# Kernel tuning notes

Measured on AMD Instinct MI355X. Metric: run time of the kernel, lower is better.

The kernel has to match this reference:

```python
import jax, jax.numpy as jnp
import numpy as np

B, S, D, H, F, V, T, L = 64, 1024, 256, 256, 128, 50000, 64, 8
H2 = 2 * H
DIN = H2 + D + 3 * F  # 1152


def setup_inputs() -> dict:
    key = jax.random.key(0)
    ks = jax.random.split(key, 12)
    sd = 0.05
    return {
        "word_ids": jax.random.randint(ks[0], (B, S), 1, V, dtype=jnp.int32),
        "embed": jax.random.normal(ks[1], (V, D), jnp.float32) * sd,
        "encoder_outputs": jax.random.normal(ks[2], (B, S, H2), jnp.float32) * sd,
        "wconv1": jax.random.normal(ks[3], (F, 1, D), jnp.float32) * sd,
        "bconv1": jax.random.normal(ks[4], (F,), jnp.float32) * sd,
        "wconv2": jax.random.normal(ks[5], (F, 2, D), jnp.float32) * sd,
        "bconv2": jax.random.normal(ks[6], (F,), jnp.float32) * sd,
        "wconv3": jax.random.normal(ks[7], (F, 3, D), jnp.float32) * sd,
        "bconv3": jax.random.normal(ks[8], (F,), jnp.float32) * sd,
        "W_ih": jax.random.normal(ks[9], (4 * H2, DIN), jnp.float32) * sd,
        "W_hh": jax.random.normal(ks[10], (4 * H2, H2), jnp.float32) * sd,
        "W_fc": jax.random.normal(ks[11], (T, H2), jnp.float32) * sd,
        "seg_len": L,
    }


def reference(word_ids, embed, encoder_outputs, wconv1, bconv1, wconv2, bconv2,
              wconv3, bconv3, W_ih, W_hh, W_fc, seg_len):
    b, s = word_ids.shape
    d = embed.shape[1]
    h2 = encoder_outputs.shape[-1]
    h = h2 // 2
    nseg = s // seg_len

    # word features via embedding lookup (WordFeature with single 'word' feature)
    wf = embed[word_ids]                                  # [B, S, D]
    xs = wf.reshape(b, nseg, seg_len, d)                  # [B, nseg, L, D]
    c_w = xs.mean(axis=2)                                 # [B, nseg, D]
    es = encoder_outputs.reshape(b, nseg, seg_len, h2)
    c_h = es.mean(axis=2)                                 # [B, nseg, 2H]

    # char-CNN per segment: conv2d(1->F, (fs, D)) == 1D conv over time with D in-channels
    xc = xs.reshape(b * nseg, seg_len, d).transpose(0, 2, 1)  # [N, D, L]

    def conv_pool(w, bias):
        k = w.transpose(0, 2, 1)                          # [F, D, fs]
        y = jax.lax.conv_general_dilated(xc, k, window_strides=(1,),
                                         padding="VALID",
                                         dimension_numbers=("NCH", "OIH", "NCH"))
        y = jax.nn.relu(y + bias[None, :, None])
        return y.max(axis=2)                              # max-pool over time -> [N, F]

    c_x = jnp.concatenate([conv_pool(wconv1, bconv1),
                           conv_pool(wconv2, bconv2),
                           conv_pool(wconv3, bconv3)], axis=1)
    c_x = c_x.reshape(b, nseg, -1)                        # [B, nseg, 3F]

    dec_in = jnp.concatenate([c_w, c_h, c_x], axis=-1)    # [B, nseg, DIN]

    # decoder init: fwd-last / bwd-first encoder states
    h0 = jnp.concatenate([encoder_outputs[:, -1, :h], encoder_outputs[:, 0, h:]], axis=1)
    c0 = jnp.zeros_like(h0)

    def step(carry, x):
        hh, cc = carry
        gates = x @ W_ih.T + hh @ W_hh.T                  # [B, 4*2H]
        i, fg, g, o = jnp.split(gates, 4, axis=1)
        cc = jax.nn.sigmoid(fg) * cc + jax.nn.sigmoid(i) * jnp.tanh(g)
        hh = jax.nn.sigmoid(o) * jnp.tanh(cc)
        out = jax.nn.log_softmax(hh @ W_fc.T, axis=-1)
        return (hh, cc), out

    _, outs = jax.lax.scan(step, (h0, c0), dec_in.transpose(1, 0, 2))  # [nseg, B, T]
    return outs.transpose(1, 0, 2).reshape(b * nseg, -1)  # batch-major like the torch loop
```

## Files before the change

kernel.cpp:

```cpp
#include <hip/hip_runtime.h>
#include <math.h>

#define BB   64
#define SS   1024
#define DD   256
#define H2   512
#define FF   128
#define TT   64
#define NSEG 128
#define DIN  1152
#define G4   2048
#define MROWS 8192
#define MX   65536

typedef __attribute__((ext_vector_type(8))) short bf16x8;
typedef __attribute__((ext_vector_type(4))) float f32x4;

__device__ __forceinline__ unsigned short f2b(float f){
    union { float f; unsigned u; } v; v.f = f;
    unsigned r = v.u + 0x7fffu + ((v.u >> 16) & 1u);
    return (unsigned short)(r >> 16);
}
__device__ __forceinline__ float b2f(unsigned short h){
    union { unsigned u; float f; } v; v.u = ((unsigned)h) << 16;
    return v.f;
}


__global__ void k_cvt(const float* __restrict__ src, unsigned short* __restrict__ dst, int n){
    int i = blockIdx.x * 256 + threadIdx.x;
    if (i < n) dst[i] = f2b(src[i]);
}

__global__ void k_wf(const float* __restrict__ w1, const float* __restrict__ w2,
                     const float* __restrict__ w3, unsigned short* __restrict__ Wf){
    int i = blockIdx.x * 256 + threadIdx.x;
    int col = i >> 8, d = i & 255;
    float v;
    if (col < 128)      v = w1[col * 256 + d];
    else if (col < 384) { int f = (col - 128) & 127; int tap = (col - 128) >> 7; v = w2[f * 512 + tap * 256 + d]; }
    else                { int c = col - 384; int f = c & 127; int tap = c >> 7;  v = w3[f * 768 + tap * 256 + d]; }
    Wf[i] = f2b(v);
}

__global__ void k_tr_wfc(const float* __restrict__ src, float* __restrict__ dst){
    int i = blockIdx.x * 256 + threadIdx.x;
    int v = i >> 9, k = i & 511;
    dst[k * 64 + v] = src[i];
}

__global__ void k_gather(const int* __restrict__ wid, const float* __restrict__ embed,
                         unsigned short* __restrict__ X){
    int i = blockIdx.x * 256 + threadIdx.x;
    int row = i >> 6, d4 = i & 63;
    int w = wid[row];
    float4 v = *(const float4*)(embed + (size_t)w * DD + d4 * 4);
    ushort4 o; o.x = f2b(v.x); o.y = f2b(v.y); o.z = f2b(v.z); o.w = f2b(v.w);
    *(ushort4*)(X + (size_t)row * DD + d4 * 4) = o;
}

__global__ void k_cw(const unsigned short* __restrict__ X, unsigned short* __restrict__ dec){
    int i = blockIdx.x * 256 + threadIdx.x;
    int row = i >> 8, d = i & 255;
    const unsigned short* p = X + (size_t)row * 8 * DD + d;
    float s = 0.f;
#pragma unroll
    for (int t = 0; t < 8; t++) s += b2f(p[t * DD]);
    dec[(size_t)row * DIN + d] = f2b(s * 0.125f);
}

__global__ void k_ch(const float* __restrict__ enc, unsigned short* __restrict__ dec){
    int i = blockIdx.x * 256 + threadIdx.x;
    int row = i >> 9, c = i & 511;
    const float* p = enc + (size_t)row * 8 * H2 + c;
    float s = 0.f;
#pragma unroll
    for (int t = 0; t < 8; t++) s += p[t * H2];
    dec[(size_t)row * DIN + 256 + c] = f2b(s * 0.125f);
}

__global__ void k_h0(const float* __restrict__ enc, unsigned short* __restrict__ Hbuf){
    int i = blockIdx.x * 256 + threadIdx.x;
    int b = i >> 9, c = i & 511;
    float v = (c < 256) ? enc[(size_t)b * SS * H2 + (size_t)(SS - 1) * H2 + c]
                        : enc[(size_t)b * SS * H2 + c];
    Hbuf[(size_t)(c >> 3) * 512 + b * 8 + (c & 7)] = f2b(v);
}

__global__ __launch_bounds__(256) void gemm_bt(
    const unsigned short* __restrict__ A, const unsigned short* __restrict__ Bm,
    unsigned short* __restrict__ C, int M, int N, int K)
{
    __shared__ unsigned short As[128][40];
    __shared__ unsigned short Bs[128][40];
    const int tid = threadIdx.x;
    const int m0 = blockIdx.y * 128, n0 = blockIdx.x * 128;
    const int w = tid >> 6, lane = tid & 63;
    const int lm = lane & 15, quad = lane >> 4;
    const int wm = (w >> 1) * 64, wn = (w & 1) * 64;

    const f32x4 z = {0.f, 0.f, 0.f, 0.f};
    f32x4 acc[4][4];
#pragma unroll
    for (int i = 0; i < 4; i++)
#pragma unroll
        for (int j = 0; j < 4; j++) acc[i][j] = z;

    const int r0 = tid >> 2;
    const int kp = (tid & 3) * 8;

    for (int kc = 0; kc < K; kc += 32){
        uint4 a0 = *(const uint4*)(A + (size_t)(m0 + r0) * K + kc + kp);
        uint4 a1 = *(const uint4*)(A + (size_t)(m0 + 64 + r0) * K + kc + kp);
        uint4 b0 = *(const uint4*)(Bm + (size_t)(n0 + r0) * K + kc + kp);
        uint4 b1 = *(const uint4*)(Bm + (size_t)(n0 + 64 + r0) * K + kc + kp);
        __syncthreads();
        *(uint4*)&As[r0][kp] = a0;
        *(uint4*)&As[64 + r0][kp] = a1;
        *(uint4*)&Bs[r0][kp] = b0;
        *(uint4*)&Bs[64 + r0][kp] = b1;
        __syncthreads();
        bf16x8 af[4], bf[4];
#pragma unroll
        for (int mt = 0; mt < 4; mt++) af[mt] = *(const bf16x8*)&As[wm + mt * 16 + lm][quad * 8];
#pragma unroll
        for (int nt = 0; nt < 4; nt++) bf[nt] = *(const bf16x8*)&Bs[wn + nt * 16 + lm][quad * 8];
#pragma unroll
        for (int mt = 0; mt < 4; mt++)
#pragma unroll
            for (int nt = 0; nt < 4; nt++)
                acc[mt][nt] = __builtin_amdgcn_mfma_f32_16x16x32_bf16(af[mt], bf[nt], acc[mt][nt], 0, 0, 0);
    }
#pragma unroll
    for (int mt = 0; mt < 4; mt++){
        int mrow = m0 + wm + mt * 16 + quad * 4;
#pragma unroll
        for (int nt = 0; nt < 4; nt++){
            int ncol = n0 + wn + nt * 16 + lm;
#pragma unroll
            for (int r = 0; r < 4; r++)
                C[(size_t)(mrow + r) * N + ncol] = f2b(acc[mt][nt][r]);
        }
    }
}

__global__ __launch_bounds__(256) void gemm_bt_gates(
    const unsigned short* __restrict__ A, const unsigned short* __restrict__ Bm,
    unsigned short* __restrict__ C, int M, int N, int K)
{
    __shared__ unsigned short As[128][40];
    __shared__ unsigned short Bs[128][40];
    const int tid = threadIdx.x;
    const int m0 = blockIdx.y * 128, n0 = blockIdx.x * 128;
    const int w = tid >> 6, lane = tid & 63;
    const int lm = lane & 15, quad = lane >> 4;
    const int wm = (w >> 1) * 64, wn = (w & 1) * 64;

    const f32x4 z = {0.f, 0.f, 0.f, 0.f};
    f32x4 acc[4][4];
#pragma unroll
    for (int i = 0; i < 4; i++)
#pragma unroll
        for (int j = 0; j < 4; j++) acc[i][j] = z;

    const int r0 = tid >> 2;
    const int kp = (tid & 3) * 8;

    for (int kc = 0; kc < K; kc += 32){
        uint4 a0 = *(const uint4*)(A + (size_t)(m0 + r0) * K + kc + kp);
        uint4 a1 = *(const uint4*)(A + (size_t)(m0 + 64 + r0) * K + kc + kp);
        uint4 b0 = *(const uint4*)(Bm + (size_t)(n0 + r0) * K + kc + kp);
        uint4 b1 = *(const uint4*)(Bm + (size_t)(n0 + 64 + r0) * K + kc + kp);
        __syncthreads();
        *(uint4*)&As[r0][kp] = a0;
        *(uint4*)&As[64 + r0][kp] = a1;
        *(uint4*)&Bs[r0][kp] = b0;
        *(uint4*)&Bs[64 + r0][kp] = b1;
        __syncthreads();
        bf16x8 af[4], bf[4];
#pragma unroll
        for (int mt = 0; mt < 4; mt++) af[mt] = *(const bf16x8*)&As[wm + mt * 16 + lm][quad * 8];
#pragma unroll
        for (int nt = 0; nt < 4; nt++) bf[nt] = *(const bf16x8*)&Bs[wn + nt * 16 + lm][quad * 8];
#pragma unroll
        for (int mt = 0; mt < 4; mt++)
#pragma unroll
            for (int nt = 0; nt < 4; nt++)
                acc[mt][nt] = __builtin_amdgcn_mfma_f32_16x16x32_bf16(af[mt], bf[nt], acc[mt][nt], 0, 0, 0);
    }
#pragma unroll
    for (int mt = 0; mt < 4; mt++){
        int mrow = m0 + wm + mt * 16 + quad * 4;
#pragma unroll
        for (int nt = 0; nt < 4; nt++){
            int ncol = n0 + wn + nt * 16 + lm;
            int cb = (ncol >> 3) & 63, g = ncol >> 9, j = ncol & 7;
#pragma unroll
            for (int r = 0; r < 4; r++){
                int m = mrow + r;
                int b = m >> 7, t = m & 127;
                size_t dst = ((((size_t)cb * NSEG + t) * 64 + b) * 4 + g) * 8 + j;
                C[dst] = f2b(acc[mt][nt][r]);
            }
        }
    }
}

__global__ void k_pool(const unsigned short* __restrict__ G, const float* __restrict__ bias,
                       unsigned short* __restrict__ dec, int taps, int colofs){
    int i = blockIdx.x * 256 + threadIdx.x;
    int row = i >> 7, f = i & 127;
    int N = taps * 128;
    float mx = -1e30f;
    for (int t = 0; t <= 8 - taps; t++){
        float a = 0.f;
        for (int tap = 0; tap < taps; tap++)
            a += b2f(G[(size_t)(row * 8 + t + tap) * N + tap * 128 + f]);
        mx = fmaxf(mx, a);
    }
    mx = fmaxf(mx + bias[f], 0.f);
    dec[(size_t)row * DIN + 768 + colofs + f] = f2b(mx);
}

__global__ __launch_bounds__(256, 1) void k_lstm(
    const unsigned short* __restrict__ gxt,
    const unsigned short* __restrict__ Whh,
    unsigned short* __restrict__ Hbuf,
    int* flags)
{
    __shared__ unsigned short Wl[32][520];
    const int tid = threadIdx.x;
    const int cb = blockIdx.x;
    const int c0 = cb * 8;
    const int w = tid >> 6, lane = tid & 63, lm = lane & 15, quad = lane >> 4;

#pragma unroll
    for (int i = 0; i < 8; i++){
        int u = tid + i * 256;
        int r = u >> 6, k8 = (u & 63) * 8;
        int g = r >> 3, c = r & 7;
        *(uint4*)&Wl[r][k8] = *(const uint4*)(Whh + (size_t)(g * H2 + c0 + c) * H2 + k8);
    }
    __syncthreads();

    float cst[4] = {0.f, 0.f, 0.f, 0.f};

    for (int t = 0; t < NSEG; t++){
        float pre[4][4];
        if (lm < 8){
            const unsigned short* gp = gxt + ((size_t)cb * NSEG + t) * 2048
                                           + (w * 16 + quad * 4) * 32 + lm;
#pragma unroll
            for (int r = 0; r < 4; r++)
#pragma unroll
                for (int g = 0; g < 4; g++)
                    pre[r][g] = b2f(gp[r * 32 + g * 8]);
        }

        if (t > 0){
            if (w == 0){
                int* fp = flags + (t - 1) * 64 + lane;
                while (!__hip_atomic_load(fp, __ATOMIC_RELAXED, __HIP_MEMORY_SCOPE_AGENT))
                    __builtin_amdgcn_s_sleep(1);
            }
            __syncthreads();
        }

        const unsigned short* hp = Hbuf + (size_t)t * (BB * H2);
        f32x4 acc0 = {0.f,0.f,0.f,0.f}, acc1 = {0.f,0.f,0.f,0.f};
#pragma unroll
        for (int ks = 0; ks < 16; ks++){
            const unsigned long long* ap =
                (const unsigned long long*)(hp + (size_t)(ks * 4 + quad) * 512 + (w * 16 + lm) * 8);
            union { unsigned long long q[2]; bf16x8 v; } u;
            u.q[0] = __hip_atomic_load(ap,     __ATOMIC_RELAXED, __HIP_MEMORY_SCOPE_AGENT);
            u.q[1] = __hip_atomic_load(ap + 1, __ATOMIC_RELAXED, __HIP_MEMORY_SCOPE_AGENT);
            bf16x8 av = u.v;
            bf16x8 b0 = *(const bf16x8*)&Wl[lm][ks * 32 + quad * 8];
            bf16x8 b1 = *(const bf16x8*)&Wl[16 + lm][ks * 32 + quad * 8];
            acc0 = __builtin_amdgcn_mfma_f32_16x16x32_bf16(av, b0, acc0, 0, 0, 0);
            acc1 = __builtin_amdgcn_mfma_f32_16x16x32_bf16(av, b1, acc1, 0, 0, 0);
        }
        float p0[4], p1[4];
#pragma unroll
        for (int r = 0; r < 4; r++){
            p0[r] = __shfl_xor(acc0[r], 8);
            p1[r] = __shfl_xor(acc1[r], 8);
        }
        if (lm < 8){
            unsigned short* hwbase = Hbuf + (size_t)(t + 1) * (BB * H2) + (size_t)cb * 512;
#pragma unroll
            for (int r = 0; r < 4; r++){
                int b = w * 16 + quad * 4 + r;
                float iv = acc0[r] + pre[r][0];
                float fv = p0[r]   + pre[r][1];
                float gv = acc1[r] + pre[r][2];
                float ov = p1[r]   + pre[r][3];
                float si = 1.f / (1.f + expf(-iv));
                float sf = 1.f / (1.f + expf(-fv));
                float so = 1.f / (1.f + expf(-ov));
                cst[r] = sf * cst[r] + si * tanhf(gv);
                unsigned short hv16 = f2b(so * tanhf(cst[r]));
                unsigned short prt = (unsigned short)__shfl_xor((int)hv16, 1);
                if (!(lm & 1)){
                    unsigned int packed = (unsigned)hv16 | ((unsigned)prt << 16);
                    __hip_atomic_store((unsigned int*)(hwbase + b * 8 + lm), packed,
                                       __ATOMIC_RELAXED, __HIP_MEMORY_SCOPE_AGENT);
                }
            }
        }
        __syncthreads();
        if (tid == 0)
            __hip_atomic_store(flags + t * 64 + cb, 1, __ATOMIC_RELAXED, __HIP_MEMORY_SCOPE_AGENT);
    }
}

__global__ __launch_bounds__(256) void k_out(
    const unsigned short* __restrict__ Hbuf, const float* __restrict__ Wt, float* __restrict__ out)
{
    __shared__ float hsh[4][H2];
    const int w = threadIdx.x >> 6, lane = threadIdx.x & 63;
    const int row = blockIdx.x * 4 + w;
    const int b = row >> 7, t = row & 127;
    const unsigned short* hp = Hbuf + (size_t)(t + 1) * (BB * H2) + b * 8;
    uint4 hv = *(const uint4*)(hp + (size_t)lane * 512);
    const unsigned short* hs = (const unsigned short*)&hv;
#pragma unroll
    for (int i = 0; i < 8; i++) hsh[w][lane * 8 + i] = b2f(hs[i]);
    __syncthreads();
    float acc = 0.f;
#pragma unroll 8
    for (int k = 0; k < H2; k++)
        acc = fmaf(hsh[w][k], Wt[k * 64 + lane], acc);
    float m = acc;
#pragma unroll
    for (int off = 32; off; off >>= 1) m = fmaxf(m, __shfl_xor(m, off));
    float e = expf(acc - m), s = e;
#pragma unroll
    for (int off = 32; off; off >>= 1) s += __shfl_xor(s, off);
    out[(size_t)row * TT + lane] = acc - m - logf(s);
}

extern "C" void kernel_launch(void* const* d_in, const int* in_sizes, int n_in,
                              void* d_out, int out_size, void* d_ws, size_t ws_size,
                              hipStream_t stream)
{
    const int*   wid = (const int*)d_in[0];
    const float* emb = (const float*)d_in[1];
    const float* enc = (const float*)d_in[2];
    const float* wc1 = (const float*)d_in[3];
    const float* bc1 = (const float*)d_in[4];
    const float* wc2 = (const float*)d_in[5];
    const float* bc2 = (const float*)d_in[6];
    const float* wc3 = (const float*)d_in[7];
    const float* bc3 = (const float*)d_in[8];
    const float* wih = (const float*)d_in[9];
    const float* whh = (const float*)d_in[10];
    const float* wfc = (const float*)d_in[11];

    char* ws = (char*)d_ws;
    size_t off = 0;
    auto alloc = [&](size_t bytes) -> void* {
        void* p = ws + off; off += (bytes + 255) & ~(size_t)255; return p;
    };
    unsigned short* X    = (unsigned short*)alloc((size_t)MX * DD * 2);
    unsigned short* dec  = (unsigned short*)alloc((size_t)MROWS * DIN * 2);
    unsigned short* Gb   = (unsigned short*)alloc((size_t)MX * 384 * 2);
    unsigned short* Wfb  = (unsigned short*)alloc((size_t)768 * 256 * 2);
    unsigned short* Wihb = (unsigned short*)alloc((size_t)G4 * DIN * 2);
    unsigned short* Whhb = (unsigned short*)alloc((size_t)G4 * H2 * 2);
    float*          Wfct = (float*)alloc((size_t)H2 * TT * 4);
    int*            flags = (int*)alloc((size_t)NSEG * 64 * 4);
    unsigned short* Hbuf  = X;
    unsigned short* gates = Gb;

    hipMemsetAsync(flags, 0, (size_t)NSEG * 64 * 4, stream);
    k_cvt<<<(G4 * DIN + 255) / 256, 256, 0, stream>>>(wih, Wihb, G4 * DIN);
    k_cvt<<<(G4 * H2 + 255) / 256, 256, 0, stream>>>(whh, Whhb, G4 * H2);
    k_wf<<<768, 256, 0, stream>>>(wc1, wc2, wc3, Wfb);
    k_tr_wfc<<<128, 256, 0, stream>>>(wfc, Wfct);
    k_gather<<<MX / 4, 256, 0, stream>>>(wid, emb, X);
    k_cw<<<MROWS, 256, 0, stream>>>(X, dec);
    k_ch<<<MROWS * 2, 256, 0, stream>>>(enc, dec);

    gemm_bt<<<dim3(1, 512), 256, 0, stream>>>(X, Wfb,                         Gb, MX, 128, 256);
    k_pool<<<4096, 256, 0, stream>>>(Gb, bc1, dec, 1, 0);
    gemm_bt<<<dim3(2, 512), 256, 0, stream>>>(X, Wfb + (size_t)128 * 256,     Gb, MX, 256, 256);
    k_pool<<<4096, 256, 0, stream>>>(Gb, bc2, dec, 2, 128);
    gemm_bt<<<dim3(3, 512), 256, 0, stream>>>(X, Wfb + (size_t)384 * 256,     Gb, MX, 384, 256);
    k_pool<<<4096, 256, 0, stream>>>(Gb, bc3, dec, 3, 256);

    k_h0<<<BB * H2 / 256, 256, 0, stream>>>(enc, Hbuf);
    gemm_bt_gates<<<dim3(16, 64), 256, 0, stream>>>(dec, Wihb, gates, MROWS, G4, DIN);
    k_lstm<<<64, 256, 0, stream>>>(gates, Whhb, Hbuf, flags);
    k_out<<<2048, 256, 0, stream>>>(Hbuf, Wfct, (float*)d_out);
}
```

Before: 1.036 ms.

## Replace LSTM flag barrier with NaN-sentinel data polling and register-resident weights

The per-step flag array and the block-wide barrier in the recurrent LSTM kernel are removed. Each wave now polls the hidden-state data directly: the buffer is pre-filled with a bf16 NaN sentinel, and produced values with bit 0x4000 set are clamped to zero so they cannot be mistaken for the sentinel. The W_hh slice is held in registers instead of shared memory, and sigmoid/tanh switch to fast exp-based forms. The aim is to cut cross-block synchronisation latency on the serial critical path. The cost is higher register pressure and a silent accuracy change: clamping any hidden value with magnitude of roughly 2 or more to zero is harmless only because |h| stays below 1.

```diff
diff --git a/kernel.cpp b/kernel.cpp
--- a/kernel.cpp
+++ b/kernel.cpp
@@ -25,6 +25,14 @@
     union { unsigned u; float f; } v; v.u = ((unsigned)h) << 16;
     return v.f;
 }
+__device__ __forceinline__ float fsig(float x){
+    return 1.f / (1.f + __expf(-x));
+}
+__device__ __forceinline__ float ftanh(float x){
+    float e = __expf(-2.f * fabsf(x));
+    float r = (1.f - e) / (1.f + e);
+    return x < 0.f ? -r : r;
+}
 
 
 __global__ void k_cvt(const float* __restrict__ src, unsigned short* __restrict__ dst, int n){
@@ -85,6 +93,12 @@
     float v = (c < 256) ? enc[(size_t)b * SS * H2 + (size_t)(SS - 1) * H2 + c]
                         : enc[(size_t)b * SS * H2 + c];
     Hbuf[(size_t)(c >> 3) * 512 + b * 8 + (c & 7)] = f2b(v);
+}
+
+__global__ void k_fill(uint4* __restrict__ p){
+    int i = blockIdx.x * 256 + threadIdx.x;
+    uint4 v; v.x = v.y = v.z = v.w = 0x7FC07FC0u;
+    p[i] = v;
 }
 
 __global__ __launch_bounds__(256) void gemm_bt(
@@ -225,27 +239,36 @@
 __global__ __launch_bounds__(256, 1) void k_lstm(
     const unsigned short* __restrict__ gxt,
     const unsigned short* __restrict__ Whh,
-    unsigned short* __restrict__ Hbuf,
-    int* flags)
+    unsigned short* __restrict__ Hbuf)
 {
-    __shared__ unsigned short Wl[32][520];
     const int tid = threadIdx.x;
     const int cb = blockIdx.x;
     const int c0 = cb * 8;
     const int w = tid >> 6, lane = tid & 63, lm = lane & 15, quad = lane >> 4;
 
-#pragma unroll
-    for (int i = 0; i < 8; i++){
-        int u = tid + i * 256;
-        int r = u >> 6, k8 = (u & 63) * 8;
-        int g = r >> 3, c = r & 7;
-        *(uint4*)&Wl[r][k8] = *(const uint4*)(Whh + (size_t)(g * H2 + c0 + c) * H2 + k8);
-    }
-    __syncthreads();
+    bf16x8 wf0[16], wf1[16];
+    {
+        const unsigned short* w0p = Whh + (size_t)(((lm >> 3)    ) * H2 + c0 + (lm & 7)) * H2 + quad * 8;
+        const unsigned short* w1p = Whh + (size_t)(((lm >> 3) + 2) * H2 + c0 + (lm & 7)) * H2 + quad * 8;
+#pragma unroll
+        for (int ks = 0; ks < 16; ks++){
+            wf0[ks] = *(const bf16x8*)(w0p + ks * 32);
+            wf1[ks] = *(const bf16x8*)(w1p + ks * 32);
+        }
+    }
 
     float cst[4] = {0.f, 0.f, 0.f, 0.f};
 
     for (int t = 0; t < NSEG; t++){
+        const unsigned long long* bas = (const unsigned long long*)
+            (Hbuf + (size_t)t * (BB * H2) + (size_t)quad * 512 + (w * 16 + lm) * 8);
+        union HU { unsigned long long q[2]; bf16x8 v; } u[16];
+#pragma unroll
+        for (int ks = 0; ks < 16; ks++){
+            u[ks].q[0] = __hip_atomic_load(bas + (size_t)ks * 512,     __ATOMIC_RELAXED, __HIP_MEMORY_SCOPE_AGENT);
+            u[ks].q[1] = __hip_atomic_load(bas + (size_t)ks * 512 + 1, __ATOMIC_RELAXED, __HIP_MEMORY_SCOPE_AGENT);
+        }
+
         float pre[4][4];
         if (lm < 8){
             const unsigned short* gp = gxt + ((size_t)cb * NSEG + t) * 2048
@@ -257,30 +280,28 @@
                     pre[r][g] = b2f(gp[r * 32 + g * 8]);
         }
 
-        if (t > 0){
-            if (w == 0){
-                int* fp = flags + (t - 1) * 64 + lane;
-                while (!__hip_atomic_load(fp, __ATOMIC_RELAXED, __HIP_MEMORY_SCOPE_AGENT))
-                    __builtin_amdgcn_s_sleep(1);
+        unsigned pend = 0xFFFFu;
+        while (pend){
+#pragma unroll
+            for (int ks = 0; ks < 16; ks++){
+                if (pend & (1u << ks)){
+                    if (((u[ks].q[0] | u[ks].q[1]) & 0x4000400040004000ULL) == 0ULL){
+                        pend &= ~(1u << ks);
+                    } else {
+                        u[ks].q[0] = __hip_atomic_load(bas + (size_t)ks * 512,     __ATOMIC_RELAXED, __HIP_MEMORY_SCOPE_AGENT);
+                        u[ks].q[1] = __hip_atomic_load(bas + (size_t)ks * 512 + 1, __ATOMIC_RELAXED, __HIP_MEMORY_SCOPE_AGENT);
+                    }
+                }
             }
-            __syncthreads();
-        }
-
-        const unsigned short* hp = Hbuf + (size_t)t * (BB * H2);
+        }
+
         f32x4 acc0 = {0.f,0.f,0.f,0.f}, acc1 = {0.f,0.f,0.f,0.f};
 #pragma unroll
         for (int ks = 0; ks < 16; ks++){
-            const unsigned long long* ap =
-                (const unsigned long long*)(hp + (size_t)(ks * 4 + quad) * 512 + (w * 16 + lm) * 8);
-            union { unsigned long long q[2]; bf16x8 v; } u;
-            u.q[0] = __hip_atomic_load(ap,     __ATOMIC_RELAXED, __HIP_MEMORY_SCOPE_AGENT);
-            u.q[1] = __hip_atomic_load(ap + 1, __ATOMIC_RELAXED, __HIP_MEMORY_SCOPE_AGENT);
-            bf16x8 av = u.v;
-            bf16x8 b0 = *(const bf16x8*)&Wl[lm][ks * 32 + quad * 8];
-            bf16x8 b1 = *(const bf16x8*)&Wl[16 + lm][ks * 32 + quad * 8];
-            acc0 = __builtin_amdgcn_mfma_f32_16x16x32_bf16(av, b0, acc0, 0, 0, 0);
-            acc1 = __builtin_amdgcn_mfma_f32_16x16x32_bf16(av, b1, acc1, 0, 0, 0);
-        }
+            acc0 = __builtin_amdgcn_mfma_f32_16x16x32_bf16(u[ks].v, wf0[ks], acc0, 0, 0, 0);
+            acc1 = __builtin_amdgcn_mfma_f32_16x16x32_bf16(u[ks].v, wf1[ks], acc1, 0, 0, 0);
+        }
+
         float p0[4], p1[4];
 #pragma unroll
         for (int r = 0; r < 4; r++){
@@ -296,22 +317,21 @@
                 float fv = p0[r]   + pre[r][1];
                 float gv = acc1[r] + pre[r][2];
                 float ov = p1[r]   + pre[r][3];
-                float si = 1.f / (1.f + expf(-iv));
-                float sf = 1.f / (1.f + expf(-fv));
-                float so = 1.f / (1.f + expf(-ov));
-                cst[r] = sf * cst[r] + si * tanhf(gv);
-                unsigned short hv16 = f2b(so * tanhf(cst[r]));
+                float si = fsig(iv);
+                float sf = fsig(fv);
+                float so = fsig(ov);
+                cst[r] = sf * cst[r] + si * ftanh(gv);
+                unsigned short hv16 = f2b(so * ftanh(cst[r]));
+                if (hv16 & 0x4000u) hv16 = 0;
                 unsigned short prt = (unsigned short)__shfl_xor((int)hv16, 1);
                 if (!(lm & 1)){
-                    unsigned int packed = (unsigned)hv16 | ((unsigned)prt << 16);
-                    __hip_atomic_store((unsigned int*)(hwbase + b * 8 + lm), packed,
+                    unsigned packed = (unsigned)hv16 | ((unsigned)prt << 16);
+                    __hip_atomic_store((unsigned*)(hwbase + b * 8 + lm), packed,
                                        __ATOMIC_RELAXED, __HIP_MEMORY_SCOPE_AGENT);
                 }
             }
         }
-        __syncthreads();
-        if (tid == 0)
-            __hip_atomic_store(flags + t * 64 + cb, 1, __ATOMIC_RELAXED, __HIP_MEMORY_SCOPE_AGENT);
+        asm volatile("" ::: "memory");
     }
 }
 
@@ -370,11 +390,9 @@
     unsigned short* Wihb = (unsigned short*)alloc((size_t)G4 * DIN * 2);
     unsigned short* Whhb = (unsigned short*)alloc((size_t)G4 * H2 * 2);
     float*          Wfct = (float*)alloc((size_t)H2 * TT * 4);
-    int*            flags = (int*)alloc((size_t)NSEG * 64 * 4);
     unsigned short* Hbuf  = X;
     unsigned short* gates = Gb;
 
-    hipMemsetAsync(flags, 0, (size_t)NSEG * 64 * 4, stream);
     k_cvt<<<(G4 * DIN + 255) / 256, 256, 0, stream>>>(wih, Wihb, G4 * DIN);
     k_cvt<<<(G4 * H2 + 255) / 256, 256, 0, stream>>>(whh, Whhb, G4 * H2);
     k_wf<<<768, 256, 0, stream>>>(wc1, wc2, wc3, Wfb);
@@ -391,7 +409,9 @@
     k_pool<<<4096, 256, 0, stream>>>(Gb, bc3, dec, 3, 256);
 
     k_h0<<<BB * H2 / 256, 256, 0, stream>>>(enc, Hbuf);
+    k_fill<<<2048, 256, 0, stream>>>((uint4*)(Hbuf + 32768));
+
     gemm_bt_gates<<<dim3(16, 64), 256, 0, stream>>>(dec, Wihb, gates, MROWS, G4, DIN);
-    k_lstm<<<64, 256, 0, stream>>>(gates, Whhb, Hbuf, flags);
+    k_lstm<<<64, 256, 0, stream>>>(gates, Whhb, Hbuf);
     k_out<<<2048, 256, 0, stream>>>(Hbuf, Wfct, (float*)d_out);
 }
```

New measurement: 1.387 ms. 1.34x slower.
